# Kernel optimization log

Hardware: AMD Instinct MI355X
Metric: run time of the kernel (lower is better)

## Reference

```python
import jax, jax.numpy as jnp
import numpy as np

B, C, D, H, W = 4, 256, 16, 16, 16


def setup_inputs() -> dict:
    key = jax.random.key(0)
    ks = jax.random.split(key, 9)
    s = 1.0 / np.sqrt(C)
    inp = {
        "x": jax.random.normal(ks[0], (B, C, D, H, W), dtype=jnp.float32),
        "wq": jax.random.normal(ks[1], (C, C), dtype=jnp.float32) * s,
        "bq": jax.random.normal(ks[2], (C,), dtype=jnp.float32) * 0.02,
        "wk": jax.random.normal(ks[3], (C, C), dtype=jnp.float32) * s,
        "bk": jax.random.normal(ks[4], (C,), dtype=jnp.float32) * 0.02,
        "wv": jax.random.normal(ks[5], (C, C), dtype=jnp.float32) * s,
        "bv": jax.random.normal(ks[6], (C,), dtype=jnp.float32) * 0.02,
        "wp": jax.random.normal(ks[7], (C, C), dtype=jnp.float32) * s,
        "bp": jax.random.normal(ks[8], (C,), dtype=jnp.float32) * 0.02,
    }
    return inp


def reference(x, wq, bq, wk, bk, wv, bv, wp, bp):
    b, c, d, h, w = x.shape
    xf = x.reshape(b, c, d * h * w)  # (B, C, N)
    # 1x1 Conv3d == per-voxel linear map over channels
    q = jnp.einsum('oc,bcn->bon', wq, xf) + bq[:, None]
    k = jnp.einsum('oc,bcn->bon', wk, xf) + bk[:, None]
    v = jnp.einsum('oc,bcn->bon', wv, xf) + bv[:, None]
    # scores[b,i,j] = q[:, :, i] . k[:, :, j], scaled AFTER the bmm (as in source)
    scores = jnp.einsum('bci,bcj->bij', q, k) * (c ** -0.5)
    p = jax.nn.softmax(scores, axis=2)  # (B, N, N), softmax over keys j
    # attention[b,c,i] = sum_j v[b,c,j] * p[b,i,j]
    attn = jnp.einsum('bcj,bij->bci', v, p)
    out = jnp.einsum('oc,bcn->bon', wp, attn) + bp[:, None]
    return x + out.reshape(b, c, d, h, w)
```

## Files before the change

### kernel.cpp

```cpp
#include <hip/hip_runtime.h>

typedef unsigned short u16;
typedef unsigned int u32;
typedef __bf16 v8bf __attribute__((ext_vector_type(8)));
typedef float v4f __attribute__((ext_vector_type(4)));

#define DEV __device__ __forceinline__

constexpr int CB = 4;
constexpr int C = 256;
constexpr int NN = 4096;
constexpr float LOG2E = 1.4426950408889634f;
constexpr int PST = 44;

DEV u16 f2bf(float f) {
  union { float f; u32 u; } v; v.f = f;
  u32 r = v.u + 0x7fffu + ((v.u >> 16) & 1u);
  return (u16)(r >> 16);
}
DEV float bf2f(u16 h) {
  union { u32 u; float f; } v; v.u = ((u32)h) << 16; return v.f;
}

DEV void dma16(const u16* g, const u16* lds_base) {
  __builtin_amdgcn_global_load_lds(
      (const __attribute__((address_space(1))) void*)(unsigned long long)g,
      (__attribute__((address_space(3))) void*)(u32)(unsigned long long)lds_base,
      16, 0, 0);
}

__global__ __launch_bounds__(256) void k_transpose(const float* __restrict__ x,
                                                   u16* __restrict__ xT) {
  __shared__ float tile[32][33];
  int b = blockIdx.z;
  int n0 = blockIdx.x * 32, c0 = blockIdx.y * 32;
  int tx = threadIdx.x & 31, ty = threadIdx.x >> 5;
  const float* xb = x + (long)b * C * NN;
#pragma unroll
  for (int r = 0; r < 4; ++r)
    tile[ty + r * 8][tx] = xb[(long)(c0 + ty + r * 8) * NN + n0 + tx];
  __syncthreads();
  u16* xTb = xT + (long)b * NN * C;
#pragma unroll
  for (int r = 0; r < 4; ++r)
    xTb[(long)(n0 + ty + r * 8) * C + c0 + tx] = f2bf(tile[tx][ty + r * 8]);
}

__global__ __launch_bounds__(256) void k_cvt4(const float* __restrict__ s0,
                                              const float* __restrict__ s1,
                                              const float* __restrict__ s2,
                                              const float* __restrict__ s3,
                                              u16* __restrict__ d0, u16* __restrict__ d1,
                                              u16* __restrict__ d2, u16* __restrict__ d3,
                                              float* __restrict__ Mbuf) {
  if (blockIdx.x == 0 && blockIdx.y == 0 && threadIdx.x < 8) Mbuf[threadIdx.x] = 0.f;
  int wsel = blockIdx.y;
  const float* s = wsel == 0 ? s0 : wsel == 1 ? s1 : wsel == 2 ? s2 : s3;
  u16* d = wsel == 0 ? d0 : wsel == 1 ? d1 : wsel == 2 ? d2 : d3;
  int i = blockIdx.x * 256 + threadIdx.x;
  d[i] = f2bf(s[i]);
}

DEV void stage_dma(const u16* __restrict__ g, const u16* lds, int w, int lane) {
#pragma unroll
  for (int i = 0; i < 8; ++i) {
    int idx = w * 8 + i;
    int r = idx * 2 + (lane >> 5);
    int cg = (lane & 31) ^ (r & 7);
    dma16(g + (long)r * 256 + cg * 8, lds + idx * 512);
  }
}

__global__ __launch_bounds__(256) void k_qkv(
    const u16* __restrict__ xT, const u16* __restrict__ wqb, const u16* __restrict__ wkb,
    const u16* __restrict__ wvb, const float* __restrict__ bq, const float* __restrict__ bk,
    const float* __restrict__ bv, u16* __restrict__ qO, u16* __restrict__ kO,
    u16* __restrict__ vO, float* __restrict__ Pn) {
  __shared__ __align__(16) u16 Ash[64 * 256];
  __shared__ __align__(16) u16 Bsh[64 * 256];
  int t = threadIdx.x, w = t >> 6, lane = t & 63, lr = lane & 15, q = lane >> 4;
  int m0 = blockIdx.x * 64, n0 = blockIdx.y * 64, b = blockIdx.z;
  const int xk = lr & 7;
  stage_dma(xT + (long)b * NN * C + (long)m0 * 256, Ash, w, lane);
  stage_dma(wqb + (long)n0 * 256, Bsh, w, lane);
  asm volatile("s_waitcnt vmcnt(0)\n\ts_barrier" ::: "memory");
#pragma unroll 1
  for (int wsel = 0; wsel < 3; ++wsel) {
    v4f acc[4];
#pragma unroll
    for (int nt = 0; nt < 4; ++nt)
#pragma unroll
      for (int r = 0; r < 4; ++r) acc[nt][r] = 0.f;
#pragma unroll
    for (int ks = 0; ks < 8; ++ks) {
      int cg = ((ks * 4 + q) ^ xk) << 3;
      v8bf a = *reinterpret_cast<const v8bf*>(Ash + (w * 16 + lr) * 256 + cg);
#pragma unroll
      for (int nt = 0; nt < 4; ++nt) {
        v8bf bb = *reinterpret_cast<const v8bf*>(Bsh + (nt * 16 + lr) * 256 + cg);
        acc[nt] = __builtin_amdgcn_mfma_f32_16x16x32_bf16(a, bb, acc[nt], 0, 0, 0);
      }
    }
    asm volatile("s_waitcnt lgkmcnt(0)\n\ts_barrier" ::: "memory");
    if (wsel < 2) {
      stage_dma((wsel == 0 ? wkb : wvb) + (long)n0 * 256, Bsh, w, lane);
      const float* bias = wsel == 0 ? bq : bk;
      float sn[4] = {0.f, 0.f, 0.f, 0.f};
#pragma unroll
      for (int nt = 0; nt < 4; ++nt) {
#pragma unroll
        for (int r = 0; r < 4; ++r) {
          int gm = m0 + w * 16 + q * 4 + r;
          int gn = n0 + nt * 16 + lr;
          float val = acc[nt][r] + bias[gn];
          if (wsel == 0) {
            float vs = val * (0.0625f * LOG2E);
            qO[((long)b * NN + gm) * C + gn] = f2bf(vs);
            sn[r] += vs * vs;
          } else {
            kO[((long)b * NN + gm) * C + gn] = f2bf(val);
            sn[r] += val * val;
          }
        }
      }
#pragma unroll
      for (int r = 0; r < 4; ++r) {
#pragma unroll
        for (int d = 1; d < 16; d <<= 1) sn[r] += __shfl_xor(sn[r], d, 64);
      }
      if (lr == 0) {
#pragma unroll
        for (int r = 0; r < 4; ++r)
          Pn[(((long)wsel * 4 + blockIdx.y) * CB + b) * NN + m0 + w * 16 + q * 4 + r] =
              sn[r];
      }
      asm volatile("s_waitcnt vmcnt(0)\n\ts_barrier" ::: "memory");
    } else {
      u16* Vt = Ash;
#pragma unroll
      for (int nt = 0; nt < 4; ++nt) {
#pragma unroll
        for (int r = 0; r < 4; ++r) {
          int gn_l = nt * 16 + lr;
          int gm_l = w * 16 + q * 4 + r;
          float val = acc[nt][r] + bv[n0 + gn_l];
          Vt[gn_l * 72 + gm_l] = f2bf(val);
        }
      }
      asm volatile("s_waitcnt lgkmcnt(0)\n\ts_barrier" ::: "memory");
      int row = t >> 2;
      u16* vrow = vO + (long)b * C * NN + (long)(n0 + row) * NN + m0;
#pragma unroll
      for (int s2 = 0; s2 < 2; ++s2) {
        int seg = (t & 3) * 2 + s2;
        *reinterpret_cast<uint4*>(vrow + seg * 8) =
            *reinterpret_cast<const uint4*>(Vt + row * 72 + seg * 8);
      }
    }
  }
}

__global__ __launch_bounds__(256) void k_norm(const float* __restrict__ Pn,
                                              float* __restrict__ Mbuf) {
  int tsel = blockIdx.y, b = blockIdx.z;
  float mx = 0.f;
  for (int row = threadIdx.x; row < NN; row += 256) {
    float s = 0.f;
#pragma unroll
    for (int qr = 0; qr < 4; ++qr)
      s += Pn[(((long)tsel * 4 + qr) * CB + b) * NN + row];
    mx = fmaxf(mx, s);
  }
#pragma unroll
  for (int d = 1; d < 64; d <<= 1) mx = fmaxf(mx, __shfl_xor(mx, d, 64));
  if ((threadIdx.x & 63) == 0)
    atomicMax((u32*)(Mbuf + tsel * 4 + b), __float_as_uint(mx));
}

__global__ __launch_bounds__(256) void k_gemm(
    const u16* __restrict__ A, long aStr, const u16* __restrict__ Bm, long bStr,
    const float* __restrict__ biasM, const float* __restrict__ biasN,
    const float* __restrict__ resid, long rStr, float scale,
    float* __restrict__ outF, u16* __restrict__ outH, long oStr, int ldm, int ldn) {
  __shared__ __align__(16) u16 Ash[64 * 256];
  __shared__ __align__(16) u16 Bsh[64 * 256];
  int t = threadIdx.x;
  int w = t >> 6, lane = t & 63, lr = lane & 15, q = lane >> 4;
  int m0 = blockIdx.x * 64, n0 = blockIdx.y * 64, b = blockIdx.z;
  const int xk = lr & 7;
  stage_dma(A + b * aStr + (long)m0 * 256, Ash, w, lane);
  stage_dma(Bm + b * bStr + (long)n0 * 256, Bsh, w, lane);
  asm volatile("s_waitcnt vmcnt(0)\n\ts_barrier" ::: "memory");
  v4f acc[4];
#pragma unroll
  for (int nt = 0; nt < 4; ++nt)
#pragma unroll
    for (int r = 0; r < 4; ++r) acc[nt][r] = 0.f;
#pragma unroll
  for (int ks = 0; ks < 8; ++ks) {
    int cg = ((ks * 4 + q) ^ xk) << 3;
    v8bf a = *reinterpret_cast<const v8bf*>(Ash + (w * 16 + lr) * 256 + cg);
#pragma unroll
    for (int nt = 0; nt < 4; ++nt) {
      v8bf bb = *reinterpret_cast<const v8bf*>(Bsh + (nt * 16 + lr) * 256 + cg);
      acc[nt] = __builtin_amdgcn_mfma_f32_16x16x32_bf16(a, bb, acc[nt], 0, 0, 0);
    }
  }
#pragma unroll
  for (int nt = 0; nt < 4; ++nt) {
#pragma unroll
    for (int r = 0; r < 4; ++r) {
      int gm = m0 + w * 16 + q * 4 + r;
      int gn = n0 + nt * 16 + lr;
      float val = acc[nt][r];
      if (biasM) val += biasM[gm];
      if (biasN) val += biasN[gn];
      val *= scale;
      long addr = b * oStr + (long)gm * ldm + (long)gn * ldn;
      if (resid) val += resid[b * rStr + (long)gm * ldm + (long)gn * ldn];
      if (outF) outF[addr] = val;
      else outH[addr] = f2bf(val);
    }
  }
}

DEV void kissue(const u16* kb, const u16* kshb, int j0, int w, int lane) {
#pragma unroll
  for (int i = 0; i < 4; ++i) {
    int idx = w * 4 + i;
    int kr = idx * 2 + (lane >> 5);
    int kc = (lane & 31) ^ (kr & 7);
    dma16(kb + (long)(j0 + kr) * 256 + kc * 8, kshb + idx * 512);
  }
}

#define FLASH_STEP(IT, VL, VU, PW, PR, KC, KN)                                     \
  {                                                                                \
    int jn_ = ((IT) + 1 < niter) ? jstart + (((IT) + 1) << 5) : jstart;            \
    kissue(kb, (KN), jn_, w, lane);                                                \
    asm volatile("" ::: "memory");    \
    {                                                                              \
      int jv_ = jstart + ((IT) << 5);                                              \
      _Pragma("unroll") for (int cs = 0; cs < 4; ++cs)                             \
          VL[cs] = *reinterpret_cast<const v8bf*>(                                 \
              vbw + (long)(cs * 16 + lr) * NN + jv_ + q * 8);                      \
    }                                                                              \
    v4f s0_, s1_;                                                                  \
    _Pragma("unroll") for (int r = 0; r < 4; ++r) { s0_[r] = 0.f; s1_[r] = 0.f; }  \
    _Pragma("unroll") for (int ks = 0; ks < 8; ++ks) {                             \
      int cg_ = ((ks * 4 + q) ^ xk) << 3;                                          \
      v8bf k0_ = *reinterpret_cast<const v8bf*>((KC) + lr * 256 + cg_);            \
      v8bf k1_ = *reinterpret_cast<const v8bf*>((KC) + (16 + lr) * 256 + cg_);     \
      s0_ = __builtin_amdgcn_mfma_f32_16x16x32_bf16(qf[ks], k0_, s0_, 0, 0, 0);    \
      s1_ = __builtin_amdgcn_mfma_f32_16x16x32_bf16(qf[ks], k1_, s1_, 0, 0, 0);    \
    }                                                                              \
    _Pragma("unroll") for (int r = 0; r < 4; ++r) {                                \
      float p0_ = exp2f(s0_[r] - M);                                               \
      float p1_ = exp2f(s1_[r] - M);                                               \
      lsum[r] += p0_ + p1_;                                                        \
      (PW)[(q * 4 + r) * PST + lr] = (u16)((__float_as_uint(p0_) + 0x8000u) >> 16);\
      (PW)[(q * 4 + r) * PST + 16 + lr] =                                          \
          (u16)((__float_as_uint(p1_) + 0x8000u) >> 16);                           \
    }                                                                              \
    if ((IT) > 0) {                                                                \
      v8bf pa_[4];                                                                 \
      _Pragma("unroll") for (int qs = 0; qs < 4; ++qs)                             \
          pa_[qs] = *reinterpret_cast<const v8bf*>(                                \
              (PR) + (qs * 16 + lr) * PST + q * 8);                                \
      _Pragma("unroll") for (int cs = 0; cs < 4; ++cs)                             \
        _Pragma("unroll") for (int qs = 0; qs < 4; ++qs)                           \
          accO[qs * 4 + cs] = __builtin_amdgcn_mfma_f32_16x16x32_bf16(             \
              pa_[qs], VU[cs], accO[qs * 4 + cs], 0, 0, 0);                        \
    }                                                                              \
    asm volatile("s_waitcnt vmcnt(4) lgkmcnt(0)\n\ts_barrier" ::: "memory");       \
  }

__global__ __launch_bounds__(256, 2) void k_flash(const u16* __restrict__ qT,
                                                  const u16* __restrict__ kT,
                                                  const u16* __restrict__ V,
                                                  u16* __restrict__ op0,
                                                  u16* __restrict__ op1,
                                                  u16* __restrict__ op2,
                                                  u16* __restrict__ op3,
                                                  float* __restrict__ ml,
                                                  const float* __restrict__ Mbuf,
                                                  int span) {
  __shared__ __align__(16) u16 ksh[2][32 * 256];
  __shared__ __align__(16) u16 psh[2][64 * PST];
  int t = threadIdx.x;
  int w = t >> 6, lane = t & 63, lr = lane & 15, q = lane >> 4;
  int total = gridDim.x * gridDim.y * gridDim.z;
  int flat = blockIdx.x + gridDim.x * (blockIdx.y + gridDim.y * blockIdx.z);
  int nf = (flat & 7) * (total >> 3) + (flat >> 3);
  int h = (nf >> 6) & (gridDim.y - 1);
  int b = nf >> (6 + __builtin_ctz(gridDim.y));
  int i0 = (nf & 63) * 64;
  const u16* qb = qT + ((long)b * NN + i0 + w * 16) * C;
  const u16* kb = kT + (long)b * NN * C;
  const u16* vbw = V + (long)b * C * NN + (long)(w * 64) * NN;
  float M = sqrtf(Mbuf[b] * Mbuf[4 + b]) + 1.5f;

  v8bf qf[8];
#pragma unroll
  for (int ks = 0; ks < 8; ++ks)
    qf[ks] = *reinterpret_cast<const v8bf*>(qb + lr * C + ks * 32 + q * 8);

  v4f accO[16];
#pragma unroll
  for (int ct = 0; ct < 16; ++ct)
#pragma unroll
    for (int r = 0; r < 4; ++r) accO[ct][r] = 0.f;
  float lsum[4] = {0.f, 0.f, 0.f, 0.f};

  u16* pw0 = psh[0] + w * 16 * PST;
  u16* pw1 = psh[1] + w * 16 * PST;
  const int xk = lr & 7;

  int jstart = h * span;
  int niter = span >> 5;

  kissue(kb, ksh[0], jstart, w, lane);
  asm volatile("s_waitcnt vmcnt(0)\n\ts_barrier" ::: "memory");

  v8bf vA[4] = {}, vB[4] = {};
#pragma unroll 1
  for (int it2 = 0; it2 < niter; it2 += 2) {
    FLASH_STEP(it2,     vA, vB, pw0, psh[1], ksh[0], ksh[1])
    FLASH_STEP(it2 + 1, vB, vA, pw1, psh[0], ksh[1], ksh[0])
  }
  {
    v8bf pa_[4];
#pragma unroll
    for (int qs = 0; qs < 4; ++qs)
      pa_[qs] = *reinterpret_cast<const v8bf*>(psh[1] + (qs * 16 + lr) * PST + q * 8);
#pragma unroll
    for (int cs = 0; cs < 4; ++cs)
#pragma unroll
      for (int qs = 0; qs < 4; ++qs)
        accO[qs * 4 + cs] = __builtin_amdgcn_mfma_f32_16x16x32_bf16(
            pa_[qs], vB[cs], accO[qs * 4 + cs], 0, 0, 0);
  }

#pragma unroll
  for (int r = 0; r < 4; ++r) {
#pragma unroll
    for (int d = 1; d < 16; d <<= 1) lsum[r] += __shfl_xor(lsum[r], d, 64);
  }
  u16* opp = h == 0 ? op0 : h == 1 ? op1 : h == 2 ? op2 : op3;
  u16* ob = opp + ((long)b * NN + i0) * C;
#pragma unroll
  for (int qs = 0; qs < 4; ++qs)
#pragma unroll
    for (int cs = 0; cs < 4; ++cs)
#pragma unroll
      for (int r = 0; r < 4; ++r)
        ob[(qs * 16 + q * 4 + r) * C + w * 64 + cs * 16 + lr] =
            f2bf(accO[qs * 4 + cs][r]);
  if (lr == 0) {
    long rbase = ((long)h * CB + b) * NN + i0 + w * 16 + q * 4;
#pragma unroll
    for (int r = 0; r < 4; ++r) {
      ml[(rbase + r) * 2] = M;
      ml[(rbase + r) * 2 + 1] = lsum[r];
    }
  }
}

__global__ __launch_bounds__(256) void k_combine(const u16* __restrict__ p0,
                                                 const u16* __restrict__ p1,
                                                 const u16* __restrict__ p2,
                                                 const u16* __restrict__ p3,
                                                 const float* __restrict__ ml,
                                                 u16* __restrict__ o, int js) {
  long row = (long)blockIdx.x * 8 + (threadIdx.x >> 5);
  int tc = (threadIdx.x & 31) * 8;
  float m[4], l[4];
  float mx = -3.0e38f;
  for (int h = 0; h < js; ++h) {
    m[h] = ml[((long)h * CB * NN + row) * 2];
    l[h] = ml[((long)h * CB * NN + row) * 2 + 1];
    mx = fmaxf(mx, m[h]);
  }
  float tot = 0.f, a[4];
  for (int h = 0; h < js; ++h) { a[h] = exp2f(m[h] - mx); tot += a[h] * l[h]; }
  float inv = 1.f / tot;
  float acc[8];
#pragma unroll
  for (int i = 0; i < 8; ++i) acc[i] = 0.f;
  const u16* ps[4] = {p0, p1, p2, p3};
  for (int h = 0; h < js; ++h) {
    uint4 u = *reinterpret_cast<const uint4*>(ps[h] + row * C + tc);
    const u16* p = reinterpret_cast<const u16*>(&u);
    float wgt = a[h] * inv;
#pragma unroll
    for (int i = 0; i < 8; ++i) acc[i] += wgt * bf2f(p[i]);
  }
  u16 outv[8];
#pragma unroll
  for (int i = 0; i < 8; ++i) outv[i] = f2bf(acc[i]);
  *reinterpret_cast<uint4*>(o + row * C + tc) = *reinterpret_cast<const uint4*>(outv);
}

extern "C" void kernel_launch(void* const* d_in, const int* in_sizes, int n_in,
                              void* d_out, int out_size, void* d_ws, size_t ws_size,
                              hipStream_t stream) {
  const float* x = (const float*)d_in[0];
  const float* wq = (const float*)d_in[1];
  const float* bq = (const float*)d_in[2];
  const float* wk = (const float*)d_in[3];
  const float* bk = (const float*)d_in[4];
  const float* wv = (const float*)d_in[5];
  const float* bv = (const float*)d_in[6];
  const float* wp = (const float*)d_in[7];
  const float* bp = (const float*)d_in[8];
  float* out = (float*)d_out;
  char* ws = (char*)d_ws;

  const long SLOT = 8388608L;
  const size_t NEED4 = 524288UL + 7 * 8388608UL + 524288UL + 4096UL;
  int js = (ws_size >= NEED4) ? 4 : 2;

  u16* wqb = (u16*)(ws + 0);
  u16* wkb = (u16*)(ws + 131072L);
  u16* wvb = (u16*)(ws + 262144L);
  u16* wpb = (u16*)(ws + 393216L);
  char* base = ws + 524288L;
  u16* xT  = (u16*)(base);
  u16* qTw = (u16*)(base + 1 * SLOT);
  u16* kTw = (u16*)(base + 2 * SLOT);
  u16* vw  = (u16*)(base + 3 * SLOT);
  u16* op1 = (u16*)(base + 4 * SLOT);
  u16* op2 = js == 4 ? (u16*)(base + 5 * SLOT) : op1;
  u16* op3 = js == 4 ? (u16*)(base + 6 * SLOT) : op1;
  float* ml = (float*)(base + (js == 4 ? 7 : 5) * SLOT);
  float* Mbuf = ml + 131072;
  u16* op0 = xT;
  u16* oW  = qTw;
  float* Pn = (float*)op1;

  k_cvt4<<<dim3(256, 4), 256, 0, stream>>>(wq, wk, wv, wp, wqb, wkb, wvb, wpb, Mbuf);
  k_transpose<<<dim3(128, 8, CB), 256, 0, stream>>>(x, xT);
  k_qkv<<<dim3(64, 4, CB), 256, 0, stream>>>(xT, wqb, wkb, wvb, bq, bk, bv, qTw, kTw,
                                             vw, Pn);
  k_norm<<<dim3(1, 2, CB), 256, 0, stream>>>(Pn, Mbuf);
  k_flash<<<dim3(64, js, CB), 256, 0, stream>>>(qTw, kTw, vw, op0, op1, op2, op3, ml,
                                                Mbuf, NN / js);
  k_combine<<<2048, 256, 0, stream>>>(op0, op1, op2, op3, ml, oW, js);

  long nc = (long)NN * C;
  k_gemm<<<dim3(4, 64, CB), 256, 0, stream>>>(wpb, 0, oW, nc, bp, nullptr, x, nc,
                                              1.0f, out, nullptr, nc, NN, 1);
}
```

Baseline: 246.0 us.

## Fuse split-KV combine into output projection GEMM and fix split count at two

Removes the separate combine kernel: the projection GEMM now loads both partial attention outputs, normalizes them by the summed row sums, and stages them into shared memory before the MFMA loop. The flash kernel is always launched with two key splits, and its QK^T loop is split into two independent accumulator chains with s_setprio raised around the MFMA blocks. This cuts one launch and a full intermediate round trip through global memory. In exchange, staging is done with regular loads instead of DMA, the two-way split gives less parallelism than four, and the combine assumes both splits share the same global max M, so it skips the exp2 rescaling.

```diff
diff --git a/kernel.cpp b/kernel.cpp
--- a/kernel.cpp
+++ b/kernel.cpp
@@ -177,53 +177,6 @@
     atomicMax((u32*)(Mbuf + tsel * 4 + b), __float_as_uint(mx));
 }
 
-__global__ __launch_bounds__(256) void k_gemm(
-    const u16* __restrict__ A, long aStr, const u16* __restrict__ Bm, long bStr,
-    const float* __restrict__ biasM, const float* __restrict__ biasN,
-    const float* __restrict__ resid, long rStr, float scale,
-    float* __restrict__ outF, u16* __restrict__ outH, long oStr, int ldm, int ldn) {
-  __shared__ __align__(16) u16 Ash[64 * 256];
-  __shared__ __align__(16) u16 Bsh[64 * 256];
-  int t = threadIdx.x;
-  int w = t >> 6, lane = t & 63, lr = lane & 15, q = lane >> 4;
-  int m0 = blockIdx.x * 64, n0 = blockIdx.y * 64, b = blockIdx.z;
-  const int xk = lr & 7;
-  stage_dma(A + b * aStr + (long)m0 * 256, Ash, w, lane);
-  stage_dma(Bm + b * bStr + (long)n0 * 256, Bsh, w, lane);
-  asm volatile("s_waitcnt vmcnt(0)\n\ts_barrier" ::: "memory");
-  v4f acc[4];
-#pragma unroll
-  for (int nt = 0; nt < 4; ++nt)
-#pragma unroll
-    for (int r = 0; r < 4; ++r) acc[nt][r] = 0.f;
-#pragma unroll
-  for (int ks = 0; ks < 8; ++ks) {
-    int cg = ((ks * 4 + q) ^ xk) << 3;
-    v8bf a = *reinterpret_cast<const v8bf*>(Ash + (w * 16 + lr) * 256 + cg);
-#pragma unroll
-    for (int nt = 0; nt < 4; ++nt) {
-      v8bf bb = *reinterpret_cast<const v8bf*>(Bsh + (nt * 16 + lr) * 256 + cg);
-      acc[nt] = __builtin_amdgcn_mfma_f32_16x16x32_bf16(a, bb, acc[nt], 0, 0, 0);
-    }
-  }
-#pragma unroll
-  for (int nt = 0; nt < 4; ++nt) {
-#pragma unroll
-    for (int r = 0; r < 4; ++r) {
-      int gm = m0 + w * 16 + q * 4 + r;
-      int gn = n0 + nt * 16 + lr;
-      float val = acc[nt][r];
-      if (biasM) val += biasM[gm];
-      if (biasN) val += biasN[gn];
-      val *= scale;
-      long addr = b * oStr + (long)gm * ldm + (long)gn * ldn;
-      if (resid) val += resid[b * rStr + (long)gm * ldm + (long)gn * ldn];
-      if (outF) outF[addr] = val;
-      else outH[addr] = f2bf(val);
-    }
-  }
-}
-
 DEV void kissue(const u16* kb, const u16* kshb, int j0, int w, int lane) {
 #pragma unroll
   for (int i = 0; i < 4; ++i) {
@@ -245,15 +198,26 @@
           VL[cs] = *reinterpret_cast<const v8bf*>(                                 \
               vbw + (long)(cs * 16 + lr) * NN + jv_ + q * 8);                      \
     }                                                                              \
-    v4f s0_, s1_;                                                                  \
-    _Pragma("unroll") for (int r = 0; r < 4; ++r) { s0_[r] = 0.f; s1_[r] = 0.f; }  \
-    _Pragma("unroll") for (int ks = 0; ks < 8; ++ks) {                             \
-      int cg_ = ((ks * 4 + q) ^ xk) << 3;                                          \
-      v8bf k0_ = *reinterpret_cast<const v8bf*>((KC) + lr * 256 + cg_);            \
-      v8bf k1_ = *reinterpret_cast<const v8bf*>((KC) + (16 + lr) * 256 + cg_);     \
-      s0_ = __builtin_amdgcn_mfma_f32_16x16x32_bf16(qf[ks], k0_, s0_, 0, 0, 0);    \
-      s1_ = __builtin_amdgcn_mfma_f32_16x16x32_bf16(qf[ks], k1_, s1_, 0, 0, 0);    \
+    v4f s0a_, s0b_, s1a_, s1b_;                                                    \
+    _Pragma("unroll") for (int r = 0; r < 4; ++r) {                                \
+      s0a_[r] = 0.f; s0b_[r] = 0.f; s1a_[r] = 0.f; s1b_[r] = 0.f;                  \
     }                                                                              \
+    __builtin_amdgcn_s_setprio(1);                                                 \
+    _Pragma("unroll") for (int ks = 0; ks < 4; ++ks) {                             \
+      int cgA_ = ((ks * 4 + q) ^ xk) << 3;                                         \
+      int cgB_ = (((ks + 4) * 4 + q) ^ xk) << 3;                                   \
+      v8bf k0a_ = *reinterpret_cast<const v8bf*>((KC) + lr * 256 + cgA_);          \
+      v8bf k1a_ = *reinterpret_cast<const v8bf*>((KC) + (16 + lr) * 256 + cgA_);   \
+      v8bf k0b_ = *reinterpret_cast<const v8bf*>((KC) + lr * 256 + cgB_);          \
+      v8bf k1b_ = *reinterpret_cast<const v8bf*>((KC) + (16 + lr) * 256 + cgB_);   \
+      s0a_ = __builtin_amdgcn_mfma_f32_16x16x32_bf16(qf[ks], k0a_, s0a_, 0, 0, 0); \
+      s1a_ = __builtin_amdgcn_mfma_f32_16x16x32_bf16(qf[ks], k1a_, s1a_, 0, 0, 0); \
+      s0b_ = __builtin_amdgcn_mfma_f32_16x16x32_bf16(qf[ks + 4], k0b_, s0b_, 0, 0, 0); \
+      s1b_ = __builtin_amdgcn_mfma_f32_16x16x32_bf16(qf[ks + 4], k1b_, s1b_, 0, 0, 0); \
+    }                                                                              \
+    __builtin_amdgcn_s_setprio(0);                                                 \
+    v4f s0_ = s0a_ + s0b_;                                                         \
+    v4f s1_ = s1a_ + s1b_;                                                         \
     _Pragma("unroll") for (int r = 0; r < 4; ++r) {                                \
       float p0_ = exp2f(s0_[r] - M);                                               \
       float p1_ = exp2f(s1_[r] - M);                                               \
@@ -267,10 +231,12 @@
       _Pragma("unroll") for (int qs = 0; qs < 4; ++qs)                             \
           pa_[qs] = *reinterpret_cast<const v8bf*>(                                \
               (PR) + (qs * 16 + lr) * PST + q * 8);                                \
+      __builtin_amdgcn_s_setprio(1);                                               \
       _Pragma("unroll") for (int cs = 0; cs < 4; ++cs)                             \
         _Pragma("unroll") for (int qs = 0; qs < 4; ++qs)                           \
           accO[qs * 4 + cs] = __builtin_amdgcn_mfma_f32_16x16x32_bf16(             \
               pa_[qs], VU[cs], accO[qs * 4 + cs], 0, 0, 0);                        \
+      __builtin_amdgcn_s_setprio(0);                                               \
     }                                                                              \
     asm volatile("s_waitcnt vmcnt(4) lgkmcnt(0)\n\ts_barrier" ::: "memory");       \
   }
@@ -280,8 +246,6 @@
                                                   const u16* __restrict__ V,
                                                   u16* __restrict__ op0,
                                                   u16* __restrict__ op1,
-                                                  u16* __restrict__ op2,
-                                                  u16* __restrict__ op3,
                                                   float* __restrict__ ml,
                                                   const float* __restrict__ Mbuf,
                                                   int span) {
@@ -346,7 +310,7 @@
 #pragma unroll
     for (int d = 1; d < 16; d <<= 1) lsum[r] += __shfl_xor(lsum[r], d, 64);
   }
-  u16* opp = h == 0 ? op0 : h == 1 ? op1 : h == 2 ? op2 : op3;
+  u16* opp = h == 0 ? op0 : op1;
   u16* ob = opp + ((long)b * NN + i0) * C;
 #pragma unroll
   for (int qs = 0; qs < 4; ++qs)
@@ -366,39 +330,64 @@
   }
 }
 
-__global__ __launch_bounds__(256) void k_combine(const u16* __restrict__ p0,
-                                                 const u16* __restrict__ p1,
-                                                 const u16* __restrict__ p2,
-                                                 const u16* __restrict__ p3,
-                                                 const float* __restrict__ ml,
-                                                 u16* __restrict__ o, int js) {
-  long row = (long)blockIdx.x * 8 + (threadIdx.x >> 5);
-  int tc = (threadIdx.x & 31) * 8;
-  float m[4], l[4];
-  float mx = -3.0e38f;
-  for (int h = 0; h < js; ++h) {
-    m[h] = ml[((long)h * CB * NN + row) * 2];
-    l[h] = ml[((long)h * CB * NN + row) * 2 + 1];
-    mx = fmaxf(mx, m[h]);
-  }
-  float tot = 0.f, a[4];
-  for (int h = 0; h < js; ++h) { a[h] = exp2f(m[h] - mx); tot += a[h] * l[h]; }
-  float inv = 1.f / tot;
-  float acc[8];
-#pragma unroll
-  for (int i = 0; i < 8; ++i) acc[i] = 0.f;
-  const u16* ps[4] = {p0, p1, p2, p3};
-  for (int h = 0; h < js; ++h) {
-    uint4 u = *reinterpret_cast<const uint4*>(ps[h] + row * C + tc);
-    const u16* p = reinterpret_cast<const u16*>(&u);
-    float wgt = a[h] * inv;
-#pragma unroll
-    for (int i = 0; i < 8; ++i) acc[i] += wgt * bf2f(p[i]);
-  }
-  u16 outv[8];
-#pragma unroll
-  for (int i = 0; i < 8; ++i) outv[i] = f2bf(acc[i]);
-  *reinterpret_cast<uint4*>(o + row * C + tc) = *reinterpret_cast<const uint4*>(outv);
+__global__ __launch_bounds__(256) void k_gemmC(
+    const u16* __restrict__ wpb, const u16* __restrict__ p0, const u16* __restrict__ p1,
+    const float* __restrict__ ml, const float* __restrict__ bp,
+    const float* __restrict__ x, float* __restrict__ out) {
+  __shared__ __align__(16) u16 Ash[64 * 256];
+  __shared__ __align__(16) u16 Bsh[64 * 256];
+  int t = threadIdx.x;
+  int w = t >> 6, lane = t & 63, lr = lane & 15, q = lane >> 4;
+  int m0 = blockIdx.x * 64, n0 = blockIdx.y * 64, b = blockIdx.z;
+  const int xk = lr & 7;
+  const long nc = (long)NN * C;
+  stage_dma(wpb + (long)m0 * 256, Ash, w, lane);
+#pragma unroll
+  for (int i = 0; i < 8; ++i) {
+    int idx = w * 8 + i;
+    int r = idx * 2 + (lane >> 5);
+    int cg = (lane & 31) ^ (r & 7);
+    long goff = (long)b * nc + (long)(n0 + r) * 256 + cg * 8;
+    uint4 u0 = *reinterpret_cast<const uint4*>(p0 + goff);
+    uint4 u1 = *reinterpret_cast<const uint4*>(p1 + goff);
+    float l0 = ml[(((long)0 * CB + b) * NN + n0 + r) * 2 + 1];
+    float l1 = ml[(((long)1 * CB + b) * NN + n0 + r) * 2 + 1];
+    float inv = 1.0f / (l0 + l1);
+    const u16* e0 = reinterpret_cast<const u16*>(&u0);
+    const u16* e1 = reinterpret_cast<const u16*>(&u1);
+    u16 cv[8];
+#pragma unroll
+    for (int k2 = 0; k2 < 8; ++k2)
+      cv[k2] = f2bf((bf2f(e0[k2]) + bf2f(e1[k2])) * inv);
+    *reinterpret_cast<uint4*>(Bsh + idx * 512 + lane * 8) =
+        *reinterpret_cast<const uint4*>(cv);
+  }
+  asm volatile("s_waitcnt vmcnt(0) lgkmcnt(0)\n\ts_barrier" ::: "memory");
+  v4f acc[4];
+#pragma unroll
+  for (int nt = 0; nt < 4; ++nt)
+#pragma unroll
+    for (int r = 0; r < 4; ++r) acc[nt][r] = 0.f;
+#pragma unroll
+  for (int ks = 0; ks < 8; ++ks) {
+    int cg = ((ks * 4 + q) ^ xk) << 3;
+    v8bf a = *reinterpret_cast<const v8bf*>(Ash + (w * 16 + lr) * 256 + cg);
+#pragma unroll
+    for (int nt = 0; nt < 4; ++nt) {
+      v8bf bb = *reinterpret_cast<const v8bf*>(Bsh + (nt * 16 + lr) * 256 + cg);
+      acc[nt] = __builtin_amdgcn_mfma_f32_16x16x32_bf16(a, bb, acc[nt], 0, 0, 0);
+    }
+  }
+#pragma unroll
+  for (int nt = 0; nt < 4; ++nt) {
+#pragma unroll
+    for (int r = 0; r < 4; ++r) {
+      int gm = m0 + w * 16 + q * 4 + r;
+      int gn = n0 + nt * 16 + lr;
+      long addr = (long)b * nc + (long)gm * NN + gn;
+      out[addr] = acc[nt][r] + bp[gm] + x[addr];
+    }
+  }
 }
 
 extern "C" void kernel_launch(void* const* d_in, const int* in_sizes, int n_in,
@@ -417,8 +406,6 @@
   char* ws = (char*)d_ws;
 
   const long SLOT = 8388608L;
-  const size_t NEED4 = 524288UL + 7 * 8388608UL + 524288UL + 4096UL;
-  int js = (ws_size >= NEED4) ? 4 : 2;
 
   u16* wqb = (u16*)(ws + 0);
   u16* wkb = (u16*)(ws + 131072L);
@@ -430,12 +417,9 @@
   u16* kTw = (u16*)(base + 2 * SLOT);
   u16* vw  = (u16*)(base + 3 * SLOT);
   u16* op1 = (u16*)(base + 4 * SLOT);
-  u16* op2 = js == 4 ? (u16*)(base + 5 * SLOT) : op1;
-  u16* op3 = js == 4 ? (u16*)(base + 6 * SLOT) : op1;
-  float* ml = (float*)(base + (js == 4 ? 7 : 5) * SLOT);
+  float* ml = (float*)(base + 5 * SLOT);
   float* Mbuf = ml + 131072;
   u16* op0 = xT;
-  u16* oW  = qTw;
   float* Pn = (float*)op1;
 
   k_cvt4<<<dim3(256, 4), 256, 0, stream>>>(wq, wk, wv, wp, wqb, wkb, wvb, wpb, Mbuf);
@@ -443,11 +427,7 @@
   k_qkv<<<dim3(64, 4, CB), 256, 0, stream>>>(xT, wqb, wkb, wvb, bq, bk, bv, qTw, kTw,
                                              vw, Pn);
   k_norm<<<dim3(1, 2, CB), 256, 0, stream>>>(Pn, Mbuf);
-  k_flash<<<dim3(64, js, CB), 256, 0, stream>>>(qTw, kTw, vw, op0, op1, op2, op3, ml,
-                                                Mbuf, NN / js);
-  k_combine<<<2048, 256, 0, stream>>>(op0, op1, op2, op3, ml, oW, js);
-
-  long nc = (long)NN * C;
-  k_gemm<<<dim3(4, 64, CB), 256, 0, stream>>>(wpb, 0, oW, nc, bp, nullptr, x, nc,
-                                              1.0f, out, nullptr, nc, NN, 1);
-}
+  k_flash<<<dim3(64, 2, CB), 256, 0, stream>>>(qTw, kTw, vw, op0, op1, ml, Mbuf,
+                                               NN / 2);
+  k_gemmC<<<dim3(4, 64, CB), 256, 0, stream>>>(wpb, op0, op1, ml, bp, x, out);
+}
```

Result: faster. 229.6 us (-6.7%).
